# Performance work log

Hardware: AMD Instinct MI355X
Metric: run time of the kernel (lower is better)

Reference implementation:

```python
import jax, jax.numpy as jnp
import numpy as np

B, S, H, NH, E, D = 2, 2048, 1024, 16, 8, 1024
HD = H // NH
EPS = 1e-5


def act_quant(x):
    # BitNet b1.58 per-row (last axis) int8 activation quant with STE
    s = 127.0 / jnp.clip(jnp.max(jnp.abs(x), axis=-1, keepdims=True), 1e-5, None)
    q = jnp.clip(jnp.round(x * s), -128, 127) / s
    return x + jax.lax.stop_gradient(q - x)


def w_quant(w, axes=None):
    # ternary weight quant (mean-abs scale) with STE; axes=None -> whole tensor
    s = 1.0 / jnp.clip(jnp.mean(jnp.abs(w), axis=axes, keepdims=axes is not None), 1e-5, None)
    q = jnp.clip(jnp.round(w * s), -1, 1) / s
    return w + jax.lax.stop_gradient(q - w)


def bitlinear(x, w):  # x [..., I], w [O, I] (torch layout)
    return act_quant(x) @ w_quant(w).T


def rmsnorm(x, w):
    return x * jax.lax.rsqrt(jnp.mean(x * x, axis=-1, keepdims=True) + EPS) * w


def setup_inputs() -> dict:
    key = jax.random.key(0)
    ks = jax.random.split(key, 10)
    def n(k, shape, scale=0.02):
        return jax.random.normal(k, shape, jnp.float32) * scale
    return {
        "x": jax.random.normal(ks[0], (B, S, H), jnp.float32),
        "q_w": n(ks[1], (H, H)),
        "k_w": n(ks[2], (H, H)),
        "v_w": n(ks[3], (H, H)),
        "o_w": n(ks[4], (H, H)),
        "ln1_w": jnp.ones((H,), jnp.float32),
        "ln2_w": jnp.ones((H,), jnp.float32),
        "router_w": n(ks[5], (E, H)),
        "gate_w": n(ks[6], (E, D, H)),
        "up_w": n(ks[7], (E, D, H)),
        "down_w": n(ks[8], (E, H, D)),
    }


def reference(x, q_w, k_w, v_w, o_w, ln1_w, ln2_w, router_w, gate_w, up_w, down_w):
    # ---- attention (BitNet projections, manual causal softmax) ----
    residual = x
    xn = rmsnorm(x, ln1_w)
    q = bitlinear(xn, q_w).reshape(B, S, NH, HD).transpose(0, 2, 1, 3)  # [B,NH,S,HD]
    k = bitlinear(xn, k_w).reshape(B, S, NH, HD).transpose(0, 2, 1, 3)
    v = bitlinear(xn, v_w).reshape(B, S, NH, HD).transpose(0, 2, 1, 3)
    scale = 1.0 / jnp.sqrt(jnp.asarray(HD, x.dtype))
    attn = jnp.einsum('bhqd,bhkd->bhqk', q, k) * scale
    causal = jnp.triu(jnp.ones((S, S), bool), k=1)
    attn = jnp.where(causal[None, None], -jnp.inf, attn)
    attn = jax.nn.softmax(attn, axis=-1)
    h = jnp.einsum('bhqk,bhkd->bhqd', attn, v).transpose(0, 2, 1, 3).reshape(B, S, H)
    x = residual + bitlinear(h, o_w)

    # ---- top-1 MoE (BitNet experts, relu^2 glu) ----
    residual = x
    xn = rmsnorm(x, ln2_w)
    xf = xn.reshape(-1, H)                       # [T, H], T = B*S
    logits = xf @ router_w.T                     # [T, E]
    idx = jnp.argmax(logits, axis=-1)            # [T]
    onehot = jax.nn.one_hot(idx, E, dtype=x.dtype)  # [T, E]

    xq = act_quant(xf)
    gw = w_quant(gate_w, axes=(1, 2))            # per-expert ternary
    uw = w_quant(up_w, axes=(1, 2))
    dw = w_quant(down_w, axes=(1, 2))
    g = jnp.einsum('th,edh->etd', xq, gw)        # [E, T, D]
    u = jnp.einsum('th,edh->etd', xq, uw)
    hh = jnp.square(jnp.maximum(g, 0)) * u       # relu(gate)^2 * up
    o = jnp.einsum('etd,ehd->eth', act_quant(hh), dw)  # [E, T, H]
    moe = jnp.einsum('eth,te->th', o, onehot).reshape(B, S, H)

    return residual + moe
```

## Files before the change

### kernel.cpp

```cpp
#include <hip/hip_runtime.h>
#include <stdint.h>
#include <math.h>

#define NTOK 4096
#define H    1024
#define NHEAD 16
#define HD   64
#define SEQ  2048
#define NE   8
#define DDIM 1024

typedef __attribute__((ext_vector_type(4)))  int i32x4;
typedef __attribute__((ext_vector_type(16))) int i32x16;
typedef __attribute__((ext_vector_type(8)))  short bf16x8;
typedef __attribute__((ext_vector_type(4)))  float f32x4;


__device__ __forceinline__ i32x16 mfma_i8(i32x4 a, i32x4 b, i32x16 c) {
  return __builtin_amdgcn_mfma_i32_32x32x32_i8(a, b, c, 0, 0, 0);
}

__device__ __forceinline__ unsigned int f2bf(float f) {
  unsigned int u = __float_as_uint(f);
  return (u + 0x7fffu + ((u >> 16) & 1u)) >> 16;
}
__device__ __forceinline__ float bf2f(unsigned int b) {
  return __uint_as_float(b << 16);
}
__device__ __forceinline__ unsigned int f2bf2hl(float a, float b, unsigned int& lo) {
  unsigned int ha = f2bf(a), hb = f2bf(b);
  lo = f2bf(a - bf2f(ha)) | (f2bf(b - bf2f(hb)) << 16);
  return ha | (hb << 16);
}
__device__ __forceinline__ unsigned int fpair(float a) {
  unsigned int hi = f2bf(a);
  unsigned int lo = f2bf(a - bf2f(hi));
  return hi | (lo << 16);
}
__device__ __forceinline__ unsigned int ror16(unsigned int x) {
  return (x >> 16) | (x << 16);
}

__device__ __forceinline__ double bredd(double v, int op, double* tmp) {
#pragma unroll
  for (int o = 32; o; o >>= 1) {
    double w = __shfl_xor(v, o);
    v = op ? fmax(v, w) : v + w;
  }
  int wid = threadIdx.x >> 6;
  if ((threadIdx.x & 63) == 0) tmp[wid] = v;
  __syncthreads();
  double r = op ? fmax(fmax(tmp[0], tmp[1]), fmax(tmp[2], tmp[3]))
                : (tmp[0] + tmp[1] + tmp[2] + tmp[3]);
  __syncthreads();
  return r;
}

__device__ __forceinline__ int qpackd(double n0, double n1, double n2, double n3, double s) {
  int a = (int)fmin(fmax(rint(n0 * s), -128.0), 127.0);
  int b = (int)fmin(fmax(rint(n1 * s), -128.0), 127.0);
  int c = (int)fmin(fmax(rint(n2 * s), -128.0), 127.0);
  int d = (int)fmin(fmax(rint(n3 * s), -128.0), 127.0);
  return (a & 255) | ((b & 255) << 8) | ((c & 255) << 16) | ((d & 255) << 24);
}

__device__ __forceinline__ const float* wsrc(int tensor,
    const float* qw_, const float* kw_, const float* vw_, const float* ow_,
    const float* gw_, const float* uw_, const float* dw_) {
  if (tensor < 4) return tensor == 0 ? qw_ : tensor == 1 ? kw_ : tensor == 2 ? vw_ : ow_;
  if (tensor < 12) return gw_ + ((long long)(tensor - 4) << 20);
  if (tensor < 20) return uw_ + ((long long)(tensor - 12) << 20);
  return dw_ + ((long long)(tensor - 20) << 20);
}


__global__ __launch_bounds__(256) void k_absum(
    const float* qw_, const float* kw_, const float* vw_, const float* ow_,
    const float* gw_, const float* uw_, const float* dw_, double* partial) {
  __shared__ double tmp[4];
  int tensor = blockIdx.x >> 10;
  int j = ((blockIdx.x & 1023) << 10) + threadIdx.x * 4;
  const float* src = wsrc(tensor, qw_, kw_, vw_, ow_, gw_, uw_, dw_);
  float4 w = *(const float4*)(src + j);
  double v = fabs((double)w.x) + fabs((double)w.y) + fabs((double)w.z) + fabs((double)w.w);
  v = bredd(v, 0, tmp);
  if (threadIdx.x == 0) partial[blockIdx.x] = v;
}

__global__ __launch_bounds__(256) void k_wscale(const double* partial, double* wsd) {
  __shared__ double tmp[4];
  int tensor = blockIdx.x;
  const double* p = partial + (tensor << 10);
  int i = threadIdx.x * 4;
  double v = p[i] + p[i + 1] + p[i + 2] + p[i + 3];
  v = bredd(v, 0, tmp);
  if (threadIdx.x == 0) wsd[tensor] = 1.0 / fmax(v * (1.0 / 1048576.0), 1e-5);
}

__global__ __launch_bounds__(256) void k_quantw(
    const float* qw_, const float* kw_, const float* vw_, const float* ow_,
    const float* gw_, const float* uw_, const float* dw_,
    const double* wsd, int8_t* qw) {
  int tensor = blockIdx.x >> 10;
  int j = ((blockIdx.x & 1023) << 10) + threadIdx.x * 4;
  const float* src = wsrc(tensor, qw_, kw_, vw_, ow_, gw_, uw_, dw_);
  double s = wsd[tensor];
  float4 w = *(const float4*)(src + j);
  int a = (int)fmin(fmax(rint((double)w.x * s), -1.0), 1.0);
  int b = (int)fmin(fmax(rint((double)w.y * s), -1.0), 1.0);
  int c = (int)fmin(fmax(rint((double)w.z * s), -1.0), 1.0);
  int d = (int)fmin(fmax(rint((double)w.w * s), -1.0), 1.0);
  ((int*)qw)[(tensor << 18) + (j >> 2)] =
      (a & 255) | ((b & 255) << 8) | ((c & 255) << 16) | ((d & 255) << 24);
}


__global__ __launch_bounds__(256) void k_rms1(const float* X, const float* lnw,
                                              int8_t* xq, double* xsd) {
  __shared__ double tmp[4];
  int t = blockIdx.x, tid = threadIdx.x;
  float4 xv = ((const float4*)(X + (long long)t * H))[tid];
  double x0 = xv.x, x1 = xv.y, x2 = xv.z, x3 = xv.w;
  double ss = x0 * x0 + x1 * x1 + x2 * x2 + x3 * x3;
  ss = bredd(ss, 0, tmp);
  double r = 1.0 / sqrt(ss * (1.0 / 1024.0) + 1e-5);
  float4 wv = ((const float4*)lnw)[tid];
  double n0 = x0 * r * wv.x, n1 = x1 * r * wv.y, n2 = x2 * r * wv.z, n3 = x3 * r * wv.w;
  double ma = fmax(fmax(fabs(n0), fabs(n1)), fmax(fabs(n2), fabs(n3)));
  ma = bredd(ma, 1, tmp);
  double s = 127.0 / fmax(ma, 1e-5);
  ((int*)xq)[t * 256 + tid] = qpackd(n0, n1, n2, n3, s);
  if (tid == 0) xsd[t] = s;
}

__global__ __launch_bounds__(256) void k_actq(const float* X, int8_t* xq, double* xsd) {
  __shared__ double tmp[4];
  int t = blockIdx.x, tid = threadIdx.x;
  float4 xv = ((const float4*)(X + (long long)t * H))[tid];
  double x0 = xv.x, x1 = xv.y, x2 = xv.z, x3 = xv.w;
  double ma = fmax(fmax(fabs(x0), fabs(x1)), fmax(fabs(x2), fabs(x3)));
  ma = bredd(ma, 1, tmp);
  double s = 127.0 / fmax(ma, 1e-5);
  ((int*)xq)[t * 256 + tid] = qpackd(x0, x1, x2, x3, s);
  if (tid == 0) xsd[t] = s;
}


__global__ __launch_bounds__(256) void k_gemm(
    const int8_t* __restrict__ Xq, const double* __restrict__ xsd,
    const int8_t* __restrict__ W, const double* __restrict__ wsd, int widx,
    const float* __restrict__ residual, float* __restrict__ out) {
  __shared__ i32x4 Xs[4][128];
  __shared__ i32x4 Ws[4][128];
  int tid = threadIdx.x;
  int t0 = blockIdx.y * 128, n0 = blockIdx.x * 128;
  int w = tid >> 6, lane = tid & 63;
  int wm = w >> 1, wn = w & 1;
  int lrow = lane & 31, lk = lane >> 5;
  i32x16 acc[2][2];
#pragma unroll
  for (int i = 0; i < 2; i++)
#pragma unroll
    for (int j = 0; j < 2; j++)
#pragma unroll
      for (int r = 0; r < 16; r++) acc[i][j][r] = 0;

  for (int k0 = 0; k0 < 1024; k0 += 64) {
#pragma unroll
    for (int i = 0; i < 2; i++) {
      int u = tid * 2 + i;
      int row = u >> 2, kc = u & 3;
      Xs[kc][row] = *(const i32x4*)(Xq + (long long)(t0 + row) * 1024 + k0 + kc * 16);
      Ws[kc][row] = *(const i32x4*)(W  + (long long)(n0 + row) * 1024 + k0 + kc * 16);
    }
    __syncthreads();
#pragma unroll
    for (int ks = 0; ks < 2; ks++) {
      i32x4 a0 = Xs[ks * 2 + lk][wm * 64 + lrow];
      i32x4 a1 = Xs[ks * 2 + lk][wm * 64 + 32 + lrow];
      i32x4 b0 = Ws[ks * 2 + lk][wn * 64 + lrow];
      i32x4 b1 = Ws[ks * 2 + lk][wn * 64 + 32 + lrow];
      acc[0][0] = mfma_i8(a0, b0, acc[0][0]);
      acc[0][1] = mfma_i8(a0, b1, acc[0][1]);
      acc[1][0] = mfma_i8(a1, b0, acc[1][0]);
      acc[1][1] = mfma_i8(a1, b1, acc[1][1]);
    }
    __syncthreads();
  }

  double sw = wsd[widx];
#pragma unroll
  for (int i = 0; i < 2; i++) {
#pragma unroll
    for (int r = 0; r < 16; r++) {
      int trow = t0 + wm * 64 + i * 32 + (r & 3) + 8 * (r >> 2) + 4 * lk;
      double inv = 1.0 / (xsd[trow] * sw);
#pragma unroll
      for (int j = 0; j < 2; j++) {
        int n = n0 + wn * 64 + j * 32 + lrow;
        double v = (double)acc[i][j][r] * inv;
        if (residual) v += (double)residual[(long long)trow * H + n];
        out[(long long)trow * H + n] = (float)v;
      }
    }
  }
}


__global__ __launch_bounds__(256) void k_gemm3(
    const int8_t* __restrict__ Xq, const double* __restrict__ xsd,
    const int8_t* __restrict__ qw, const double* __restrict__ wsd,
    float* __restrict__ outq, float* __restrict__ outk, float* __restrict__ outv) {
  __shared__ i32x4 Xs[4][128];
  __shared__ i32x4 Ws[4][128];
  int z = blockIdx.z;
  const int8_t* W = qw + ((long long)z << 20);
  float* out = z == 0 ? outq : z == 1 ? outk : outv;
  int tid = threadIdx.x;
  int t0 = blockIdx.y * 128, n0 = blockIdx.x * 128;
  int w = tid >> 6, lane = tid & 63;
  int wm = w >> 1, wn = w & 1;
  int lrow = lane & 31, lk = lane >> 5;
  i32x16 acc[2][2];
#pragma unroll
  for (int i = 0; i < 2; i++)
#pragma unroll
    for (int j = 0; j < 2; j++)
#pragma unroll
      for (int r = 0; r < 16; r++) acc[i][j][r] = 0;

  for (int k0 = 0; k0 < 1024; k0 += 64) {
#pragma unroll
    for (int i = 0; i < 2; i++) {
      int u = tid * 2 + i;
      int row = u >> 2, kc = u & 3;
      Xs[kc][row] = *(const i32x4*)(Xq + (long long)(t0 + row) * 1024 + k0 + kc * 16);
      Ws[kc][row] = *(const i32x4*)(W  + (long long)(n0 + row) * 1024 + k0 + kc * 16);
    }
    __syncthreads();
#pragma unroll
    for (int ks = 0; ks < 2; ks++) {
      i32x4 a0 = Xs[ks * 2 + lk][wm * 64 + lrow];
      i32x4 a1 = Xs[ks * 2 + lk][wm * 64 + 32 + lrow];
      i32x4 b0 = Ws[ks * 2 + lk][wn * 64 + lrow];
      i32x4 b1 = Ws[ks * 2 + lk][wn * 64 + 32 + lrow];
      acc[0][0] = mfma_i8(a0, b0, acc[0][0]);
      acc[0][1] = mfma_i8(a0, b1, acc[0][1]);
      acc[1][0] = mfma_i8(a1, b0, acc[1][0]);
      acc[1][1] = mfma_i8(a1, b1, acc[1][1]);
    }
    __syncthreads();
  }

  double sw = wsd[z];
#pragma unroll
  for (int i = 0; i < 2; i++) {
#pragma unroll
    for (int r = 0; r < 16; r++) {
      int trow = t0 + wm * 64 + i * 32 + (r & 3) + 8 * (r >> 2) + 4 * lk;
      double inv = 1.0 / (xsd[trow] * sw);
#pragma unroll
      for (int j = 0; j < 2; j++) {
        int n = n0 + wn * 64 + j * 32 + lrow;
        out[(long long)trow * H + n] = (float)((double)acc[i][j][r] * inv);
      }
    }
  }
}


__global__ __launch_bounds__(256) void k_knorm(const float* __restrict__ K,
                                               float* __restrict__ Mk) {
  __shared__ float tmp[4];
  int bh = blockIdx.x;
  int b = bh >> 4, head = bh & 15;
  int tid = threadIdx.x;
  float mx = 0.f;
  for (int key = tid; key < SEQ; key += 256) {
    const float4* kr = (const float4*)(K + ((long long)(b * SEQ + key)) * H + head * HD);
    float s = 0.f;
#pragma unroll
    for (int i = 0; i < 16; i++) {
      float4 v = kr[i];
      s += v.x * v.x + v.y * v.y + v.z * v.z + v.w * v.w;
    }
    mx = fmaxf(mx, s);
  }
#pragma unroll
  for (int o = 32; o; o >>= 1) mx = fmaxf(mx, __shfl_xor(mx, o));
  if ((tid & 63) == 0) tmp[tid >> 6] = mx;
  __syncthreads();
  if (tid == 0)
    Mk[bh] = sqrtf(fmaxf(fmaxf(tmp[0], tmp[1]), fmaxf(tmp[2], tmp[3])));
}


__global__ __launch_bounds__(512, 4) void k_attn(
    const float* __restrict__ Q, const float* __restrict__ K,
    const float* __restrict__ V, float* __restrict__ O,
    const float* __restrict__ Mk) {
  __shared__ unsigned short Qb[64][72];
  __shared__ unsigned short Ql[64][72];
  __shared__ unsigned short Kb[64][72];
  __shared__ unsigned short Kl[64][72];
  __shared__ unsigned int   VA[64][76];
  __shared__ unsigned int   Pw[64][76];
  __shared__ float mbs[64];
  __shared__ float lred[64];
  int i = blockIdx.x;
  int hb = (i & 7) | (((i >> 3) & 3) << 3);
  int p  = ((i >> 5) & 7) | (((i >> 8) & 1) << 3);
  int head = hb & 15, b = hb >> 4;
  int tid = threadIdx.x;
  int w = tid >> 6, lane = tid & 63;
  int quad = lane >> 2, dp = lane & 3;
  int d0 = dp << 4;
  int l15 = lane & 15, lhi = lane >> 4;
  int qh = w >> 2, ks = w & 3;
  long long bh_base = ((long long)b * SEQ) * H + head * HD;
  float mkv = Mk[b * 16 + head];

  int srow = tid >> 3;
  int sd = (tid & 7) << 3;
  int wc = tid & 7;
  int vswz = (tid & 7) << 2;

  for (int ph = 0; ph < 2; ph++) {
    int g = ph ? (31 - p) : p;
    int qlo = g * 64;

    {
      const float* qg = Q + bh_base + (long long)(qlo + srow) * H + sd;
      float4 a = *(const float4*)qg;
      float4 c = *(const float4*)(qg + 4);
      uint4 phh, pll;
      phh.x = f2bf2hl(a.x * 0.125f, a.y * 0.125f, pll.x);
      phh.y = f2bf2hl(a.z * 0.125f, a.w * 0.125f, pll.y);
      phh.z = f2bf2hl(c.x * 0.125f, c.y * 0.125f, pll.z);
      phh.w = f2bf2hl(c.z * 0.125f, c.w * 0.125f, pll.w);
      *(uint4*)&Qb[srow][sd] = phh;
      *(uint4*)&Ql[srow][sd] = pll;
    }

    if (ks == 0) {
      int j0 = qh * 32 + quad * 2;
#pragma unroll
      for (int qq = 0; qq < 2; qq++) {
        int j = j0 + qq;
        const float4* qp_ = (const float4*)(Q + bh_base + (long long)(qlo + j) * H + d0);
        float ss = 0.f;
#pragma unroll
        for (int i2 = 0; i2 < 4; i2++) {
          float4 t = qp_[i2];
          ss += t.x * t.x + t.y * t.y + t.z * t.z + t.w * t.w;
        }
        ss += __shfl_xor(ss, 1);
        ss += __shfl_xor(ss, 2);
        if (dp == 0) mbs[j] = 0.125f * sqrtf(ss) * mkv;
      }
    }

    float lsum = 0.f;
    f32x4 oacc[2];
#pragma unroll
    for (int fi = 0; fi < 2; fi++)
#pragma unroll
      for (int r = 0; r < 4; r++) oacc[fi][r] = 0.f;

    __syncthreads();

    for (int t = 0; t <= g; t++) {
      {
        const float* kg = K + bh_base + (long long)(t * 64 + srow) * H + sd;
        const float* vg = V + bh_base + (long long)(t * 64 + srow) * H + sd;
        float4 ka = *(const float4*)kg;
        float4 kc = *(const float4*)(kg + 4);
        uint4 phh, pll;
        phh.x = f2bf2hl(ka.x, ka.y, pll.x);
        phh.y = f2bf2hl(ka.z, ka.w, pll.y);
        phh.z = f2bf2hl(kc.x, kc.y, pll.z);
        phh.w = f2bf2hl(kc.z, kc.w, pll.w);
        *(uint4*)&Kb[srow][sd] = phh;
        *(uint4*)&Kl[srow][sd] = pll;
        float4 va = *(const float4*)vg;
        float4 vc = *(const float4*)(vg + 4);
        int col = srow ^ vswz;
        VA[sd + 0][col] = fpair(va.x);
        VA[sd + 1][col] = fpair(va.y);
        VA[sd + 2][col] = fpair(va.z);
        VA[sd + 3][col] = fpair(va.w);
        VA[sd + 4][col] = fpair(vc.x);
        VA[sd + 5][col] = fpair(vc.y);
        VA[sd + 6][col] = fpair(vc.z);
        VA[sd + 7][col] = fpair(vc.w);
      }
      __syncthreads();

      {
        int qb = w >> 1;
#pragma unroll
        for (int kb2 = 0; kb2 < 2; kb2++) {
          int kb = (w & 1) * 2 + kb2;
          f32x4 c = {0.f, 0.f, 0.f, 0.f};
#pragma unroll
          for (int ks2 = 0; ks2 < 2; ks2++) {
            bf16x8 ah = *(const bf16x8*)&Qb[qb * 16 + l15][ks2 * 32 + lhi * 8];
            bf16x8 al = *(const bf16x8*)&Ql[qb * 16 + l15][ks2 * 32 + lhi * 8];
            bf16x8 bh = *(const bf16x8*)&Kb[kb * 16 + l15][ks2 * 32 + lhi * 8];
            bf16x8 bl = *(const bf16x8*)&Kl[kb * 16 + l15][ks2 * 32 + lhi * 8];
            c = __builtin_amdgcn_mfma_f32_16x16x32_bf16(al, bh, c, 0, 0, 0);
            c = __builtin_amdgcn_mfma_f32_16x16x32_bf16(ah, bl, c, 0, 0, 0);
            c = __builtin_amdgcn_mfma_f32_16x16x32_bf16(ah, bh, c, 0, 0, 0);
          }
#pragma unroll
          for (int r = 0; r < 4; r++)
            Pw[qb * 16 + lhi * 4 + r][kb * 16 + l15] = __float_as_uint(c[r]);
        }
      }
      __syncthreads();

      {
        float mbr = mbs[srow];
        uint4 pa = *(const uint4*)&Pw[srow][wc * 8];
        uint4 pb = *(const uint4*)&Pw[srow][wc * 8 + 4];
        float pv0 = __uint_as_float(pa.x), pv1 = __uint_as_float(pa.y);
        float pv2 = __uint_as_float(pa.z), pv3 = __uint_as_float(pa.w);
        float pv4 = __uint_as_float(pb.x), pv5 = __uint_as_float(pb.y);
        float pv6 = __uint_as_float(pb.z), pv7 = __uint_as_float(pb.w);
        int kbase = wc * 8;
        bool dg = (t == g);
        float w0 = (dg && kbase + 0 > srow) ? 0.f : __expf(pv0 - mbr);
        float w1 = (dg && kbase + 1 > srow) ? 0.f : __expf(pv1 - mbr);
        float w2 = (dg && kbase + 2 > srow) ? 0.f : __expf(pv2 - mbr);
        float w3 = (dg && kbase + 3 > srow) ? 0.f : __expf(pv3 - mbr);
        float w4 = (dg && kbase + 4 > srow) ? 0.f : __expf(pv4 - mbr);
        float w5 = (dg && kbase + 5 > srow) ? 0.f : __expf(pv5 - mbr);
        float w6 = (dg && kbase + 6 > srow) ? 0.f : __expf(pv6 - mbr);
        float w7 = (dg && kbase + 7 > srow) ? 0.f : __expf(pv7 - mbr);
        lsum += ((w0 + w1) + (w2 + w3)) + ((w4 + w5) + (w6 + w7));
        uint4 oa, ob;
        oa.x = fpair(w0); oa.y = fpair(w1); oa.z = fpair(w2); oa.w = fpair(w3);
        ob.x = fpair(w4); ob.y = fpair(w5); ob.z = fpair(w6); ob.w = fpair(w7);
        *(uint4*)&Pw[srow][wc * 8] = oa;
        *(uint4*)&Pw[srow][wc * 8 + 4] = ob;
      }
      __syncthreads();

#pragma unroll
      for (int fi = 0; fi < 2; fi++) {
        int f = w * 2 + fi;
        int q4 = f >> 2, d4 = f & 3;
#pragma unroll
        for (int c4 = 0; c4 < 4; c4++) {
          bf16x8 af = *(const bf16x8*)&Pw[q4 * 16 + l15][c4 * 16 + lhi * 4];
          int row = d4 * 16 + l15;
          int rswz = ((row >> 3) & 7) << 2;
          union { uint4 q; unsigned int u[4]; bf16x8 v; } bb, bs;
          bb.q = *(const uint4*)&VA[row][(c4 * 16 + lhi * 4) ^ rswz];
          oacc[fi] = __builtin_amdgcn_mfma_f32_16x16x32_bf16(af, bb.v, oacc[fi], 0, 0, 0);
#pragma unroll
          for (int j = 0; j < 4; j++)
            bs.u[j] = ror16(bb.u[j]);
          oacc[fi] = __builtin_amdgcn_mfma_f32_16x16x32_bf16(af, bs.v, oacc[fi], 0, 0, 0);
        }
      }
      __syncthreads();
    }

    lsum += __shfl_xor(lsum, 1);
    lsum += __shfl_xor(lsum, 2);
    lsum += __shfl_xor(lsum, 4);
    if ((lane & 7) == 0) lred[srow] = lsum;
    __syncthreads();
#pragma unroll
    for (int fi = 0; fi < 2; fi++) {
      int f = w * 2 + fi;
      int q4 = f >> 2, d4 = f & 3;
#pragma unroll
      for (int r = 0; r < 4; r++) {
        int qrow = q4 * 16 + lhi * 4 + r;
        float inv = 1.f / lred[qrow];
        O[bh_base + (long long)(qlo + qrow) * H + d4 * 16 + l15] = oacc[fi][r] * inv;
      }
    }
    __syncthreads();
  }
}


__global__ __launch_bounds__(256) void k_rms2_router(
    const float* X2, const float* lnw, const float* rw,
    int8_t* xq, double* xsd, int* eidx) {
  __shared__ double tmp[4];
  __shared__ double xn[1024];
  __shared__ double logits[8];
  int t = blockIdx.x, tid = threadIdx.x;
  float4 xv = ((const float4*)(X2 + (long long)t * H))[tid];
  double x0 = xv.x, x1 = xv.y, x2 = xv.z, x3 = xv.w;
  double ss = x0 * x0 + x1 * x1 + x2 * x2 + x3 * x3;
  ss = bredd(ss, 0, tmp);
  double r = 1.0 / sqrt(ss * (1.0 / 1024.0) + 1e-5);
  float4 wv = ((const float4*)lnw)[tid];
  double n0 = x0 * r * wv.x, n1 = x1 * r * wv.y, n2 = x2 * r * wv.z, n3 = x3 * r * wv.w;
  xn[tid * 4 + 0] = n0; xn[tid * 4 + 1] = n1;
  xn[tid * 4 + 2] = n2; xn[tid * 4 + 3] = n3;
  double ma = fmax(fmax(fabs(n0), fabs(n1)), fmax(fabs(n2), fabs(n3)));
  ma = bredd(ma, 1, tmp);
  double s = 127.0 / fmax(ma, 1e-5);
  ((int*)xq)[t * 256 + tid] = qpackd(n0, n1, n2, n3, s);
  if (tid == 0) xsd[t] = s;
  if (tid < 64) {
    int e = tid >> 3, i = tid & 7;
    const float* wr = rw + e * 1024;
    double p = 0.0;
    for (int h = i; h < 1024; h += 8) p += xn[h] * (double)wr[h];
    p += __shfl_xor(p, 1);
    p += __shfl_xor(p, 2);
    p += __shfl_xor(p, 4);
    if (i == 0) logits[e] = p;
  }
  __syncthreads();
  if (tid == 0) {
    double best = logits[0];
    int bi = 0;
    for (int e = 1; e < 8; e++)
      if (logits[e] > best) { best = logits[e]; bi = e; }
    eidx[t] = bi;
  }
}


__global__ __launch_bounds__(256) void k_route(const int* __restrict__ eidx,
                                               int* __restrict__ meta,
                                               int* __restrict__ tokidx) {
  __shared__ int cnt[8], pb[9], cur[8];
  int tid = threadIdx.x;
  if (tid < 8) cnt[tid] = 0;
  __syncthreads();
  for (int t = tid; t < NTOK; t += 256) atomicAdd(&cnt[eidx[t]], 1);
  __syncthreads();
  if (tid == 0) {
    pb[0] = 0;
    int nt = 0;
    for (int e = 0; e < 8; e++) {
      int tiles = (cnt[e] + 63) >> 6;
      for (int i = 0; i < tiles; i++) meta[1 + nt + i] = e;
      nt += tiles;
      pb[e + 1] = pb[e] + tiles * 64;
      cur[e] = pb[e];
    }
    meta[0] = nt;
  }
  __syncthreads();
  for (int s = tid; s < 4608; s += 256) tokidx[s] = -1;
  __syncthreads();
  for (int t = tid; t < NTOK; t += 256) {
    int e = eidx[t];
    int s = atomicAdd(&cur[e], 1);
    tokidx[s] = t;
  }
}


__global__ __launch_bounds__(256) void k_moe_gu(
    const int8_t* __restrict__ Xq, const double* __restrict__ xsd,
    const int8_t* __restrict__ qw, const double* __restrict__ wsd,
    const int* __restrict__ meta, const int* __restrict__ tokidx,
    float* __restrict__ hhbuf) {
  __shared__ i32x4 Xs[4][64];
  __shared__ i32x4 Wg[4][128];
  __shared__ i32x4 Wu[4][128];
  int tile = blockIdx.y;
  if (tile >= meta[0]) return;
  int e = meta[1 + tile];
  int n0 = blockIdx.x * 128;
  int s0 = tile * 64;
  int tid = threadIdx.x;
  int w = tid >> 6, lane = tid & 63;
  int lrow = lane & 31, lk = lane >> 5;
  const int8_t* Gg = qw + ((long long)(4 + e) << 20);
  const int8_t* Ug = qw + ((long long)(12 + e) << 20);
  int xrow = tid >> 2, xkc = tid & 3;
  int tokr = tokidx[s0 + xrow];
  if (tokr < 0) tokr = 0;
  i32x16 accg[2], accu[2];
#pragma unroll
  for (int i = 0; i < 2; i++)
#pragma unroll
    for (int r = 0; r < 16; r++) { accg[i][r] = 0; accu[i][r] = 0; }

  for (int k0 = 0; k0 < 1024; k0 += 64) {
    Xs[xkc][xrow] = *(const i32x4*)(Xq + (long long)tokr * 1024 + k0 + xkc * 16);
#pragma unroll
    for (int i = 0; i < 2; i++) {
      int u = tid * 2 + i;
      int row = u >> 2, kc = u & 3;
      Wg[kc][row] = *(const i32x4*)(Gg + (long long)(n0 + row) * 1024 + k0 + kc * 16);
      Wu[kc][row] = *(const i32x4*)(Ug + (long long)(n0 + row) * 1024 + k0 + kc * 16);
    }
    __syncthreads();
#pragma unroll
    for (int ks = 0; ks < 2; ks++) {
      i32x4 a0 = Xs[ks * 2 + lk][lrow];
      i32x4 a1 = Xs[ks * 2 + lk][32 + lrow];
      i32x4 bg = Wg[ks * 2 + lk][w * 32 + lrow];
      i32x4 bu = Wu[ks * 2 + lk][w * 32 + lrow];
      accg[0] = mfma_i8(a0, bg, accg[0]);
      accg[1] = mfma_i8(a1, bg, accg[1]);
      accu[0] = mfma_i8(a0, bu, accu[0]);
      accu[1] = mfma_i8(a1, bu, accu[1]);
    }
    __syncthreads();
  }

  double swg = wsd[4 + e], swu = wsd[12 + e];
  int n = n0 + w * 32 + lrow;
#pragma unroll
  for (int i = 0; i < 2; i++) {
#pragma unroll
    for (int r = 0; r < 16; r++) {
      int s = s0 + i * 32 + (r & 3) + 8 * (r >> 2) + 4 * lk;
      int tok = tokidx[s];
      if (tok < 0) continue;
      double ig = 1.0 / (xsd[tok] * swg);
      double iu = 1.0 / (xsd[tok] * swu);
      double g = (double)accg[i][r] * ig;
      double uu = (double)accu[i][r] * iu;
      double rg = fmax(g, 0.0);
      hhbuf[(long long)s * DDIM + n] = (float)(rg * rg * uu);
    }
  }
}


__global__ __launch_bounds__(256) void k_hh_actq(
    const float* __restrict__ hhbuf, const int* __restrict__ meta,
    const int* __restrict__ tokidx, int8_t* __restrict__ hq,
    double* __restrict__ hsd) {
  __shared__ double tmp[4];
  int s = blockIdx.x;
  if (s >= meta[0] * 64) return;
  int tid = threadIdx.x;
  int tok = tokidx[s];
  if (tok < 0) {
    ((int*)hq)[s * 256 + tid] = 0;
    if (tid == 0) hsd[s] = 1.0;
    return;
  }
  float4 xv = ((const float4*)(hhbuf + (long long)s * DDIM))[tid];
  double x0 = xv.x, x1 = xv.y, x2 = xv.z, x3 = xv.w;
  double ma = fmax(fmax(fabs(x0), fabs(x1)), fmax(fabs(x2), fabs(x3)));
  ma = bredd(ma, 1, tmp);
  double sc = 127.0 / fmax(ma, 1e-5);
  ((int*)hq)[s * 256 + tid] = qpackd(x0, x1, x2, x3, sc);
  if (tid == 0) hsd[s] = sc;
}


__global__ __launch_bounds__(256) void k_moe_down(
    const int8_t* __restrict__ hq, const double* __restrict__ hsd,
    const int8_t* __restrict__ qw, const double* __restrict__ wsd,
    const int* __restrict__ meta, const int* __restrict__ tokidx,
    const float* __restrict__ x2, float* __restrict__ out) {
  __shared__ i32x4 Xs[4][64];
  __shared__ i32x4 Ws[4][128];
  int tile = blockIdx.y;
  if (tile >= meta[0]) return;
  int e = meta[1 + tile];
  int n0 = blockIdx.x * 128;
  int s0 = tile * 64;
  int tid = threadIdx.x;
  int w = tid >> 6, lane = tid & 63;
  int lrow = lane & 31, lk = lane >> 5;
  const int8_t* Wp = qw + ((long long)(20 + e) << 20);
  int xrow = tid >> 2, xkc = tid & 3;
  i32x16 acc[2];
#pragma unroll
  for (int i = 0; i < 2; i++)
#pragma unroll
    for (int r = 0; r < 16; r++) acc[i][r] = 0;

  for (int k0 = 0; k0 < 1024; k0 += 64) {
    Xs[xkc][xrow] = *(const i32x4*)(hq + (long long)(s0 + xrow) * 1024 + k0 + xkc * 16);
#pragma unroll
    for (int i = 0; i < 2; i++) {
      int u = tid * 2 + i;
      int row = u >> 2, kc = u & 3;
      Ws[kc][row] = *(const i32x4*)(Wp + (long long)(n0 + row) * 1024 + k0 + kc * 16);
    }
    __syncthreads();
#pragma unroll
    for (int ks = 0; ks < 2; ks++) {
      i32x4 a0 = Xs[ks * 2 + lk][lrow];
      i32x4 a1 = Xs[ks * 2 + lk][32 + lrow];
      i32x4 b  = Ws[ks * 2 + lk][w * 32 + lrow];
      acc[0] = mfma_i8(a0, b, acc[0]);
      acc[1] = mfma_i8(a1, b, acc[1]);
    }
    __syncthreads();
  }

  double sw = wsd[20 + e];
  int n = n0 + w * 32 + lrow;
#pragma unroll
  for (int i = 0; i < 2; i++) {
#pragma unroll
    for (int r = 0; r < 16; r++) {
      int s = s0 + i * 32 + (r & 3) + 8 * (r >> 2) + 4 * lk;
      int tok = tokidx[s];
      if (tok < 0) continue;
      double inv = 1.0 / (hsd[s] * sw);
      out[(long long)tok * H + n] =
          (float)((double)x2[(long long)tok * H + n] + (double)acc[i][r] * inv);
    }
  }
}


extern "C" void kernel_launch(void* const* d_in, const int* in_sizes, int n_in,
                              void* d_out, int out_size, void* d_ws, size_t ws_size,
                              hipStream_t stream) {
  const float* x   = (const float*)d_in[0];
  const float* qw_ = (const float*)d_in[1];
  const float* kw_ = (const float*)d_in[2];
  const float* vw_ = (const float*)d_in[3];
  const float* ow_ = (const float*)d_in[4];
  const float* ln1 = (const float*)d_in[5];
  const float* ln2 = (const float*)d_in[6];
  const float* rw  = (const float*)d_in[7];
  const float* gw  = (const float*)d_in[8];
  const float* uw  = (const float*)d_in[9];
  const float* dw  = (const float*)d_in[10];
  float* out = (float*)d_out;

  uint8_t* ws = (uint8_t*)d_ws;
  double* partial = (double*)ws;
  double* wsd    = (double*)(ws + 229376);
  double* xsd    = (double*)(ws + 229600);
  int*    eidx   = (int*)(ws + 262368);
  float*  Mk     = (float*)(ws + 278752);
  int*    meta   = (int*)(ws + 278912);
  int*    tokidx = (int*)(ws + 279424);
  double* hsd    = (double*)(ws + 297856);
  int8_t* qw     = (int8_t*)(ws + (1ull << 20));
  int8_t* xq     = (int8_t*)(ws + (29ull << 20));
  float*  qbuf   = (float*)(ws + (33ull << 20));
  float*  hhbuf  = (float*)(ws + (33ull << 20));
  float*  kbuf   = (float*)(ws + (49ull << 20));
  int8_t* hq     = (int8_t*)(ws + (52ull << 20));
  float*  vbuf   = (float*)(ws + (65ull << 20));

  k_absum<<<28 * 1024, 256, 0, stream>>>(qw_, kw_, vw_, ow_, gw, uw, dw, partial);
  k_wscale<<<28, 256, 0, stream>>>(partial, wsd);
  k_quantw<<<28 * 1024, 256, 0, stream>>>(qw_, kw_, vw_, ow_, gw, uw, dw, wsd, qw);

  k_rms1<<<NTOK, 256, 0, stream>>>(x, ln1, xq, xsd);
  k_gemm3<<<dim3(8, 32, 3), 256, 0, stream>>>(xq, xsd, qw, wsd, qbuf, kbuf, vbuf);
  k_knorm<<<32, 256, 0, stream>>>(kbuf, Mk);
  k_attn<<<dim3(512), 512, 0, stream>>>(qbuf, kbuf, vbuf, qbuf, Mk);
  k_actq<<<NTOK, 256, 0, stream>>>(qbuf, xq, xsd);
  k_gemm<<<dim3(8, 32), 256, 0, stream>>>(xq, xsd, qw + (3 << 20), wsd, 3, x, vbuf);
  k_rms2_router<<<NTOK, 256, 0, stream>>>(vbuf, ln2, rw, xq, xsd, eidx);
  k_route<<<1, 256, 0, stream>>>(eidx, meta, tokidx);
  k_moe_gu<<<dim3(8, 71), 256, 0, stream>>>(xq, xsd, qw, wsd, meta, tokidx, hhbuf);
  k_hh_actq<<<4544, 256, 0, stream>>>(hhbuf, meta, tokidx, hq, hsd);
  k_moe_down<<<dim3(8, 71), 256, 0, stream>>>(hq, hsd, qw, wsd, meta, tokidx, vbuf, out);
}
```

Before: 529.7 us.

## Fuse softmax exp into QK^T epilogue and precompute per-row dequant scales

In the attention kernel, exp and causal masking are now applied directly in registers after the QK^T MFMA, with per-row partial sums kept per lane. This removes the separate pass that re-read scores from shared memory, along with one barrier per key tile, and the row sums are reduced with shuffles plus a small shared buffer. In all GEMM epilogues (qkv, o-proj, moe gate/up, down), each block now computes its per-row double-precision reciprocal scales once into shared memory, instead of every lane doing a double divide per accumulator element. The cost is an extra barrier and a little shared memory per block, and the attention change raises register pressure.

Result: faster. 497.7 us (-6.0%).

```diff
diff --git a/kernel.cpp b/kernel.cpp
--- a/kernel.cpp
+++ b/kernel.cpp
@@ -152,6 +152,7 @@
     const float* __restrict__ residual, float* __restrict__ out) {
   __shared__ i32x4 Xs[4][128];
   __shared__ i32x4 Ws[4][128];
+  __shared__ double invs[128];
   int tid = threadIdx.x;
   int t0 = blockIdx.y * 128, n0 = blockIdx.x * 128;
   int w = tid >> 6, lane = tid & 63;
@@ -189,12 +190,15 @@
   }
 
   double sw = wsd[widx];
+  if (tid < 128) invs[tid] = 1.0 / (xsd[t0 + tid] * sw);
+  __syncthreads();
 #pragma unroll
   for (int i = 0; i < 2; i++) {
 #pragma unroll
     for (int r = 0; r < 16; r++) {
-      int trow = t0 + wm * 64 + i * 32 + (r & 3) + 8 * (r >> 2) + 4 * lk;
-      double inv = 1.0 / (xsd[trow] * sw);
+      int rloc = wm * 64 + i * 32 + (r & 3) + 8 * (r >> 2) + 4 * lk;
+      int trow = t0 + rloc;
+      double inv = invs[rloc];
 #pragma unroll
       for (int j = 0; j < 2; j++) {
         int n = n0 + wn * 64 + j * 32 + lrow;
@@ -213,6 +217,7 @@
     float* __restrict__ outq, float* __restrict__ outk, float* __restrict__ outv) {
   __shared__ i32x4 Xs[4][128];
   __shared__ i32x4 Ws[4][128];
+  __shared__ double invs[128];
   int z = blockIdx.z;
   const int8_t* W = qw + ((long long)z << 20);
   float* out = z == 0 ? outq : z == 1 ? outk : outv;
@@ -253,12 +258,15 @@
   }
 
   double sw = wsd[z];
+  if (tid < 128) invs[tid] = 1.0 / (xsd[t0 + tid] * sw);
+  __syncthreads();
 #pragma unroll
   for (int i = 0; i < 2; i++) {
 #pragma unroll
     for (int r = 0; r < 16; r++) {
-      int trow = t0 + wm * 64 + i * 32 + (r & 3) + 8 * (r >> 2) + 4 * lk;
-      double inv = 1.0 / (xsd[trow] * sw);
+      int rloc = wm * 64 + i * 32 + (r & 3) + 8 * (r >> 2) + 4 * lk;
+      int trow = t0 + rloc;
+      double inv = invs[rloc];
 #pragma unroll
       for (int j = 0; j < 2; j++) {
         int n = n0 + wn * 64 + j * 32 + lrow;
@@ -306,7 +314,7 @@
   __shared__ unsigned int   VA[64][76];
   __shared__ unsigned int   Pw[64][76];
   __shared__ float mbs[64];
-  __shared__ float lred[64];
+  __shared__ float lsh[8][16];
   int i = blockIdx.x;
   int hb = (i & 7) | (((i >> 3) & 3) << 3);
   int p  = ((i >> 5) & 7) | (((i >> 8) & 1) << 3);
@@ -322,8 +330,9 @@
 
   int srow = tid >> 3;
   int sd = (tid & 7) << 3;
-  int wc = tid & 7;
   int vswz = (tid & 7) << 2;
+
+  int qb = w >> 1;
 
   for (int ph = 0; ph < 2; ph++) {
     int g = ph ? (31 - p) : p;
@@ -360,7 +369,7 @@
       }
     }
 
-    float lsum = 0.f;
+    float lp[4] = {0.f, 0.f, 0.f, 0.f};
     f32x4 oacc[2];
 #pragma unroll
     for (int fi = 0; fi < 2; fi++)
@@ -368,6 +377,10 @@
       for (int r = 0; r < 4; r++) oacc[fi][r] = 0.f;
 
     __syncthreads();
+
+    float mbr4[4];
+#pragma unroll
+    for (int r = 0; r < 4; r++) mbr4[r] = mbs[qb * 16 + lhi * 4 + r];
 
     for (int t = 0; t <= g; t++) {
       {
@@ -397,7 +410,7 @@
       __syncthreads();
 
       {
-        int qb = w >> 1;
+        bool dg = (t == g);
 #pragma unroll
         for (int kb2 = 0; kb2 < 2; kb2++) {
           int kb = (w & 1) * 2 + kb2;
@@ -412,47 +425,25 @@
             c = __builtin_amdgcn_mfma_f32_16x16x32_bf16(ah, bl, c, 0, 0, 0);
             c = __builtin_amdgcn_mfma_f32_16x16x32_bf16(ah, bh, c, 0, 0, 0);
           }
-#pragma unroll
-          for (int r = 0; r < 4; r++)
-            Pw[qb * 16 + lhi * 4 + r][kb * 16 + l15] = __float_as_uint(c[r]);
+          int colc = kb * 16 + l15;
+#pragma unroll
+          for (int r = 0; r < 4; r++) {
+            int row = qb * 16 + lhi * 4 + r;
+            float wgt = (dg && colc > row) ? 0.f : __expf(c[r] - mbr4[r]);
+            lp[r] += wgt;
+            Pw[row][colc] = fpair(wgt);
+          }
         }
       }
       __syncthreads();
 
-      {
-        float mbr = mbs[srow];
-        uint4 pa = *(const uint4*)&Pw[srow][wc * 8];
-        uint4 pb = *(const uint4*)&Pw[srow][wc * 8 + 4];
-        float pv0 = __uint_as_float(pa.x), pv1 = __uint_as_float(pa.y);
-        float pv2 = __uint_as_float(pa.z), pv3 = __uint_as_float(pa.w);
-        float pv4 = __uint_as_float(pb.x), pv5 = __uint_as_float(pb.y);
-        float pv6 = __uint_as_float(pb.z), pv7 = __uint_as_float(pb.w);
-        int kbase = wc * 8;
-        bool dg = (t == g);
-        float w0 = (dg && kbase + 0 > srow) ? 0.f : __expf(pv0 - mbr);
-        float w1 = (dg && kbase + 1 > srow) ? 0.f : __expf(pv1 - mbr);
-        float w2 = (dg && kbase + 2 > srow) ? 0.f : __expf(pv2 - mbr);
-        float w3 = (dg && kbase + 3 > srow) ? 0.f : __expf(pv3 - mbr);
-        float w4 = (dg && kbase + 4 > srow) ? 0.f : __expf(pv4 - mbr);
-        float w5 = (dg && kbase + 5 > srow) ? 0.f : __expf(pv5 - mbr);
-        float w6 = (dg && kbase + 6 > srow) ? 0.f : __expf(pv6 - mbr);
-        float w7 = (dg && kbase + 7 > srow) ? 0.f : __expf(pv7 - mbr);
-        lsum += ((w0 + w1) + (w2 + w3)) + ((w4 + w5) + (w6 + w7));
-        uint4 oa, ob;
-        oa.x = fpair(w0); oa.y = fpair(w1); oa.z = fpair(w2); oa.w = fpair(w3);
-        ob.x = fpair(w4); ob.y = fpair(w5); ob.z = fpair(w6); ob.w = fpair(w7);
-        *(uint4*)&Pw[srow][wc * 8] = oa;
-        *(uint4*)&Pw[srow][wc * 8 + 4] = ob;
-      }
-      __syncthreads();
-
 #pragma unroll
       for (int fi = 0; fi < 2; fi++) {
         int f = w * 2 + fi;
-        int q4 = f >> 2, d4 = f & 3;
+        int d4 = f & 3;
 #pragma unroll
         for (int c4 = 0; c4 < 4; c4++) {
-          bf16x8 af = *(const bf16x8*)&Pw[q4 * 16 + l15][c4 * 16 + lhi * 4];
+          bf16x8 af = *(const bf16x8*)&Pw[qb * 16 + l15][c4 * 16 + lhi * 4];
           int row = d4 * 16 + l15;
           int rswz = ((row >> 3) & 7) << 2;
           union { uint4 q; unsigned int u[4]; bf16x8 v; } bb, bs;
@@ -467,19 +458,29 @@
       __syncthreads();
     }
 
-    lsum += __shfl_xor(lsum, 1);
-    lsum += __shfl_xor(lsum, 2);
-    lsum += __shfl_xor(lsum, 4);
-    if ((lane & 7) == 0) lred[srow] = lsum;
-    __syncthreads();
+#pragma unroll
+    for (int r = 0; r < 4; r++) {
+      lp[r] += __shfl_xor(lp[r], 1);
+      lp[r] += __shfl_xor(lp[r], 2);
+      lp[r] += __shfl_xor(lp[r], 4);
+      lp[r] += __shfl_xor(lp[r], 8);
+    }
+    if (l15 == 0) {
+#pragma unroll
+      for (int r = 0; r < 4; r++) lsh[w][lhi * 4 + r] = lp[r];
+    }
+    __syncthreads();
+
 #pragma unroll
     for (int fi = 0; fi < 2; fi++) {
       int f = w * 2 + fi;
-      int q4 = f >> 2, d4 = f & 3;
+      int d4 = f & 3;
 #pragma unroll
       for (int r = 0; r < 4; r++) {
-        int qrow = q4 * 16 + lhi * 4 + r;
-        float inv = 1.f / lred[qrow];
+        int idx = lhi * 4 + r;
+        float lt = lsh[qb * 2][idx] + lsh[qb * 2 + 1][idx];
+        float inv = 1.f / lt;
+        int qrow = qb * 16 + idx;
         O[bh_base + (long long)(qlo + qrow) * H + d4 * 16 + l15] = oacc[fi][r] * inv;
       }
     }
@@ -570,6 +571,7 @@
   __shared__ i32x4 Xs[4][64];
   __shared__ i32x4 Wg[4][128];
   __shared__ i32x4 Wu[4][128];
+  __shared__ double invg[64], invu[64];
   int tile = blockIdx.y;
   if (tile >= meta[0]) return;
   int e = meta[1 + tile];
@@ -614,18 +616,24 @@
   }
 
   double swg = wsd[4 + e], swu = wsd[12 + e];
+  if (tid < 64) {
+    int tk = tokidx[s0 + tid];
+    double xs = (tk < 0) ? 1.0 : xsd[tk];
+    invg[tid] = 1.0 / (xs * swg);
+    invu[tid] = 1.0 / (xs * swu);
+  }
+  __syncthreads();
   int n = n0 + w * 32 + lrow;
 #pragma unroll
   for (int i = 0; i < 2; i++) {
 #pragma unroll
     for (int r = 0; r < 16; r++) {
-      int s = s0 + i * 32 + (r & 3) + 8 * (r >> 2) + 4 * lk;
+      int sl = i * 32 + (r & 3) + 8 * (r >> 2) + 4 * lk;
+      int s = s0 + sl;
       int tok = tokidx[s];
       if (tok < 0) continue;
-      double ig = 1.0 / (xsd[tok] * swg);
-      double iu = 1.0 / (xsd[tok] * swu);
-      double g = (double)accg[i][r] * ig;
-      double uu = (double)accu[i][r] * iu;
+      double g = (double)accg[i][r] * invg[sl];
+      double uu = (double)accu[i][r] * invu[sl];
       double rg = fmax(g, 0.0);
       hhbuf[(long long)s * DDIM + n] = (float)(rg * rg * uu);
     }
@@ -664,6 +672,7 @@
     const float* __restrict__ x2, float* __restrict__ out) {
   __shared__ i32x4 Xs[4][64];
   __shared__ i32x4 Ws[4][128];
+  __shared__ double invd[64];
   int tile = blockIdx.y;
   if (tile >= meta[0]) return;
   int e = meta[1 + tile];
@@ -701,17 +710,19 @@
   }
 
   double sw = wsd[20 + e];
+  if (tid < 64) invd[tid] = 1.0 / (hsd[s0 + tid] * sw);
+  __syncthreads();
   int n = n0 + w * 32 + lrow;
 #pragma unroll
   for (int i = 0; i < 2; i++) {
 #pragma unroll
     for (int r = 0; r < 16; r++) {
-      int s = s0 + i * 32 + (r & 3) + 8 * (r >> 2) + 4 * lk;
+      int sl = i * 32 + (r & 3) + 8 * (r >> 2) + 4 * lk;
+      int s = s0 + sl;
       int tok = tokidx[s];
       if (tok < 0) continue;
-      double inv = 1.0 / (hsd[s] * sw);
       out[(long long)tok * H + n] =
-          (float)((double)x2[(long long)tok * H + n] + (double)acc[i][r] * inv);
+          (float)((double)x2[(long long)tok * H + n] + (double)acc[i][r] * invd[sl]);
     }
   }
 }
```
